# Optimization experiments

Measured on AMD Instinct MI355X. Metric: run time of the kernel, lower is better.

## Reference

```python
import jax, jax.numpy as jnp
import numpy as np

N = 50000      # nodes
E = 800000     # edges (before self-loops)
FIN = 512      # in_channels
HID = 64       # hid_units[i]
HEADS = 8      # n_heads[i]
OUT = 40       # out_channels
NEG_SLOPE = 0.2


def setup_inputs() -> dict:
    key = jax.random.key(0)
    ks = jax.random.split(key, 16)
    d = {
        "x": jax.random.normal(ks[0], (N, FIN), dtype=jnp.float32),
        "edge_index": jax.random.randint(ks[1], (2, E), 0, N, dtype=jnp.int64),
        # layer 1: FIN -> HEADS*HID
        "W1": jax.random.normal(ks[2], (FIN, HEADS * HID), dtype=jnp.float32) * 0.05,
        "att_src1": jax.random.normal(ks[3], (HEADS, HID), dtype=jnp.float32) * 0.1,
        "att_dst1": jax.random.normal(ks[4], (HEADS, HID), dtype=jnp.float32) * 0.1,
        "b1": jnp.zeros((HEADS * HID,), dtype=jnp.float32),
        # layer 2: HEADS*HID -> HEADS*HID
        "W2": jax.random.normal(ks[5], (HEADS * HID, HEADS * HID), dtype=jnp.float32) * 0.05,
        "att_src2": jax.random.normal(ks[6], (HEADS, HID), dtype=jnp.float32) * 0.1,
        "att_dst2": jax.random.normal(ks[7], (HEADS, HID), dtype=jnp.float32) * 0.1,
        "b2": jnp.zeros((HEADS * HID,), dtype=jnp.float32),
        # output layer: HEADS*HID -> OUT, 1 head, concat=False
        "W3": jax.random.normal(ks[8], (HEADS * HID, OUT), dtype=jnp.float32) * 0.05,
        "att_src3": jax.random.normal(ks[9], (1, OUT), dtype=jnp.float32) * 0.1,
        "att_dst3": jax.random.normal(ks[10], (1, OUT), dtype=jnp.float32) * 0.1,
        "b3": jnp.zeros((OUT,), dtype=jnp.float32),
    }
    return d


def gat_conv(x, src, dst, W, a_src, a_dst, b, heads, out_ch, concat):
    # x: [N, Fin]; src/dst: [E'] (self-loops included)
    h = (x @ W).reshape(N, heads, out_ch)              # [N, H, C]
    alpha_src = jnp.sum(h * a_src[None], axis=-1)      # [N, H]
    alpha_dst = jnp.sum(h * a_dst[None], axis=-1)      # [N, H]
    e = jax.nn.leaky_relu(alpha_src[src] + alpha_dst[dst], NEG_SLOPE)  # [E', H]
    # segment softmax over edges grouped by target node
    m = jax.ops.segment_max(e, dst, num_segments=N)    # [N, H]
    ex = jnp.exp(e - m[dst])
    denom = jax.ops.segment_sum(ex, dst, num_segments=N)
    alpha = ex / denom[dst]                            # [E', H]
    out = jax.ops.segment_sum(h[src] * alpha[:, :, None], dst, num_segments=N)  # [N, H, C]
    out = out.reshape(N, heads * out_ch) if concat else out.mean(axis=1)
    return out + b


def reference(x, edge_index, W1, att_src1, att_dst1, b1,
              W2, att_src2, att_dst2, b2,
              W3, att_src3, att_dst3, b3):
    loop = jnp.arange(N, dtype=edge_index.dtype)
    src = jnp.concatenate([edge_index[0], loop])  # add_self_loops=True (PyG default)
    dst = jnp.concatenate([edge_index[1], loop])
    h = gat_conv(x, src, dst, W1, att_src1, att_dst1, b1, HEADS, HID, True)
    h = jax.nn.elu(h)  # dropout p=0.0 / eval -> identity
    h = gat_conv(h, src, dst, W2, att_src2, att_dst2, b2, HEADS, HID, True)
    h = jax.nn.elu(h)
    h = gat_conv(h, src, dst, W3, att_src3, att_dst3, b3, 1, OUT, False)
    return jax.nn.log_softmax(h, axis=1)
```

## Files before the change

### kernel.cpp

```cpp
#include <hip/hip_runtime.h>
#include <math.h>

#define NNODES 50000
#define NEDGES 800000
#define FINCH 512
#define HIDC 64
#define NHEADS 8
#define OUTC 40
#define NSLOPE 0.2f
#define NSB ((NNODES + 255) / 256)

typedef unsigned short ushort;
typedef unsigned int uint;
typedef __attribute__((ext_vector_type(8))) short bf16x8;
typedef __attribute__((ext_vector_type(4))) float f32x4;

static __device__ __forceinline__ float leaky(float e) { return e > 0.f ? e : NSLOPE * e; }

static __device__ __forceinline__ float bf2f(ushort u) {
    union { unsigned int i; float f; } c; c.i = ((unsigned int)u) << 16; return c.f;
}
static __device__ __forceinline__ ushort f2bf(float f) {
    union { float f; unsigned int i; } c; c.f = f;
    unsigned int r = c.i + 0x7FFF + ((c.i >> 16) & 1);
    return (ushort)(r >> 16);
}
static __device__ __forceinline__ uint fkey(float f) {
    uint u = __float_as_uint(f);
    return (u & 0x80000000u) ? ~u : (u | 0x80000000u);
}
static __device__ __forceinline__ float fdec(uint k) {
    return __uint_as_float((k & 0x80000000u) ? (k & 0x7fffffffu) : ~k);
}

static __device__ __forceinline__ void gload16(const ushort* g, ushort* l) {
    __builtin_amdgcn_global_load_lds((const __attribute__((address_space(1))) void*)g,
                                     (__attribute__((address_space(3))) void*)l, 16, 0, 0);
}

__global__ __launch_bounds__(64) void k_detect(const int* __restrict__ ei, int* __restrict__ flag,
                                               uint* __restrict__ keys) {
    int lane = threadIdx.x;
    if (lane < 17) keys[lane] = fkey(-3.0e38f);
    int v = ei[2 * lane + 1];
    unsigned long long b = __ballot(v != 0);
    if (lane == 0) *flag = (b == 0ULL) ? 1 : 0;
}

static __device__ __forceinline__ int load_idx(const int* ei, int wide, int pos) {
    int v = wide ? ei[2 * (long long)pos] : ei[pos];
    v = v < 0 ? 0 : (v >= NNODES ? NNODES - 1 : v);
    return v;
}

__global__ void k_init_deg(int* __restrict__ deg) {
    int i = blockIdx.x * blockDim.x + threadIdx.x;
    if (i < NNODES) deg[i] = 1;
}

__global__ void k_count(const int* __restrict__ ei, const int* __restrict__ flag, int* __restrict__ deg) {
    int e = blockIdx.x * blockDim.x + threadIdx.x;
    if (e < NEDGES) {
        int d = load_idx(ei, *flag, NEDGES + e);
        atomicAdd(&deg[d], 1);
    }
}

__global__ __launch_bounds__(256) void k_bsum(const int* __restrict__ deg, int* __restrict__ bsum) {
    int i = blockIdx.x * 256 + threadIdx.x;
    int v = (i < NNODES) ? deg[i] : 0;
#pragma unroll
    for (int m = 32; m > 0; m >>= 1) v += __shfl_xor(v, m);
    __shared__ int ws[4];
    int wid = threadIdx.x >> 6, lane = threadIdx.x & 63;
    if (lane == 0) ws[wid] = v;
    __syncthreads();
    if (threadIdx.x == 0) bsum[blockIdx.x] = ws[0] + ws[1] + ws[2] + ws[3];
}

__global__ __launch_bounds__(64) void k_bscan(const int* __restrict__ bsum, int* __restrict__ bofs,
                                              int* __restrict__ offs) {
    const int lane = threadIdx.x;
    const int CH = (NSB + 63) / 64;
    int lo = lane * CH, hi = min(lo + CH, NSB);
    int s = 0;
    for (int i = lo; i < hi; i++) s += bsum[i];
    int x = s;
#pragma unroll
    for (int st = 1; st < 64; st <<= 1) { int v = __shfl_up(x, st); if (lane >= st) x += v; }
    int run = x - s;
    for (int i = lo; i < hi; i++) { bofs[i] = run; run += bsum[i]; }
    if (lane == 63) offs[NNODES] = run;
}

__global__ __launch_bounds__(256) void k_scan_final(const int* __restrict__ deg, const int* __restrict__ bofs,
                                                    int* __restrict__ offs, int* __restrict__ cur) {
    int b = blockIdx.x;
    int i = b * 256 + threadIdx.x;
    int v = (i < NNODES) ? deg[i] : 0;
    int lane = threadIdx.x & 63, wid = threadIdx.x >> 6;
    int x = v;
#pragma unroll
    for (int st = 1; st < 64; st <<= 1) { int t = __shfl_up(x, st); if (lane >= st) x += t; }
    __shared__ int ws[4];
    if (lane == 63) ws[wid] = x;
    __syncthreads();
    int wofs = 0;
#pragma unroll
    for (int w = 0; w < 4; w++) if (w < wid) wofs += ws[w];
    int excl = bofs[b] + wofs + x - v;
    if (i < NNODES) { offs[i] = excl; cur[i] = excl; }
}

__global__ void k_fill(const int* __restrict__ ei, const int* __restrict__ flag,
                       int* __restrict__ cur, int* __restrict__ csr) {
    int e = blockIdx.x * blockDim.x + threadIdx.x;
    if (e < NEDGES + NNODES) {
        int s, d;
        if (e < NEDGES) {
            int w = *flag;
            s = load_idx(ei, w, e);
            d = load_idx(ei, w, NEDGES + e);
        } else {
            s = e - NEDGES; d = s;
        }
        int pos = atomicAdd(&cur[d], 1);
        csr[pos] = s;
    }
}

template <int NH>
__global__ __launch_bounds__(256) void k_msrc(const float* __restrict__ src, uint* __restrict__ keys, int n) {
    float m = -3.0e38f;
    for (int i = blockIdx.x * 256 + threadIdx.x; i < n; i += gridDim.x * 256)
        m = fmaxf(m, src[i]);
    __shared__ float red[256];
    red[threadIdx.x] = m;
    __syncthreads();
    for (int st = 128; st >= NH; st >>= 1) {
        if (threadIdx.x < st) red[threadIdx.x] = fmaxf(red[threadIdx.x], red[threadIdx.x + st]);
        __syncthreads();
    }
    if (threadIdx.x < NH) atomicMax(&keys[threadIdx.x], fkey(red[threadIdx.x]));
}

__global__ void k_f2bf(const float* __restrict__ in, ushort* __restrict__ out, int n4) {
    int i = blockIdx.x * blockDim.x + threadIdx.x;
    if (i < n4) {
        float4 v = ((const float4*)in)[i];
        ushort4 o = make_ushort4(f2bf(v.x), f2bf(v.y), f2bf(v.z), f2bf(v.w));
        ((ushort4*)out)[i] = o;
    }
}

__global__ __launch_bounds__(256) void k_transpose(const float* __restrict__ W, ushort* __restrict__ Wt) {
    __shared__ float tile[32][33];
    int bx = blockIdx.x, by = blockIdx.y;
    int tx = threadIdx.x & 31, ty = threadIdx.x >> 5;
#pragma unroll
    for (int i = 0; i < 4; i++)
        tile[ty + i * 8][tx] = W[(size_t)(by * 32 + ty + i * 8) * 512 + bx * 32 + tx];
    __syncthreads();
#pragma unroll
    for (int i = 0; i < 4; i++)
        Wt[(size_t)(bx * 32 + ty + i * 8) * 512 + by * 32 + tx] = f2bf(tile[tx][ty + i * 8]);
}

__global__ __launch_bounds__(256) void k_transpose3(const float* __restrict__ W3, ushort* __restrict__ Wt3) {
    int idx = blockIdx.x * 256 + threadIdx.x;
    int c = idx >> 9, k = idx & 511;
    Wt3[idx] = (c < OUTC) ? f2bf(W3[(size_t)k * OUTC + c]) : 0;
}

__global__ __launch_bounds__(512) void mfma_gemm2(const ushort* __restrict__ A, const ushort* __restrict__ Bt,
                                                  ushort* __restrict__ C, int M) {
    __shared__ ushort Abuf[2][128 * 32];
    __shared__ ushort Bbuf[2][128 * 32];
    const int nwg = gridDim.x;
    const int q = nwg >> 3, r = nwg & 7;
    const int orig = blockIdx.x;
    const int xcd = orig & 7, ii = orig >> 3;
    const int wgid = (xcd < r ? xcd * (q + 1) : r * (q + 1) + (xcd - r) * q) + ii;
    const int row0 = (wgid >> 2) * 128, col0 = (wgid & 3) * 128;

    const int t = threadIdx.x;
    const int wid = t >> 6, lane = t & 63;
    const int wr = wid >> 1, wc = wid & 1;
    const int l15 = lane & 15, l4 = lane >> 4;
    const int arow = t >> 2, kb = t & 3;
    const int swz = (arow >> 1) & 3;
    const int ra = min(row0 + arow, M - 1);
    const ushort* gA = A + (size_t)ra * 512 + ((kb ^ swz) << 3);
    const ushort* gB = Bt + (size_t)(col0 + arow) * 512 + ((kb ^ swz) << 3);
    f32x4 acc[2][4] = {};

    gload16(gA, &Abuf[0][wid * 512]);
    gload16(gB, &Bbuf[0][wid * 512]);
    __syncthreads();
    int cur = 0;
    for (int k0 = 0; k0 < 512; k0 += 32) {
        if (k0 + 32 < 512) {
            gload16(gA + k0 + 32, &Abuf[cur ^ 1][wid * 512]);
            gload16(gB + k0 + 32, &Bbuf[cur ^ 1][wid * 512]);
        }
        bf16x8 af[2], bfr[4];
#pragma unroll
        for (int mr = 0; mr < 2; mr++) {
            int rr = wr * 32 + mr * 16 + l15;
            af[mr] = *(const bf16x8*)&Abuf[cur][rr * 32 + ((l4 ^ ((rr >> 1) & 3)) << 3)];
        }
#pragma unroll
        for (int nr = 0; nr < 4; nr++) {
            int cc = wc * 64 + nr * 16 + l15;
            bfr[nr] = *(const bf16x8*)&Bbuf[cur][cc * 32 + ((l4 ^ ((cc >> 1) & 3)) << 3)];
        }
#pragma unroll
        for (int mr = 0; mr < 2; mr++)
#pragma unroll
            for (int nr = 0; nr < 4; nr++)
                acc[mr][nr] = __builtin_amdgcn_mfma_f32_16x16x32_bf16(af[mr], bfr[nr], acc[mr][nr], 0, 0, 0);
        __syncthreads();
        cur ^= 1;
    }
#pragma unroll
    for (int mr = 0; mr < 2; mr++) {
#pragma unroll
        for (int qq = 0; qq < 4; qq++) {
            int gr = row0 + wr * 32 + mr * 16 + l4 * 4 + qq;
            if (gr >= M) continue;
#pragma unroll
            for (int nr = 0; nr < 4; nr++) {
                int gc = col0 + wc * 64 + nr * 16 + l15;
                C[(size_t)gr * 512 + gc] = f2bf(acc[mr][nr][qq]);
            }
        }
    }
}

__global__ __launch_bounds__(256) void mfma_gemm3(const ushort* __restrict__ A, const ushort* __restrict__ Wt3,
                                                  float* __restrict__ h3, int M) {
    __shared__ ushort Abuf[2][64 * 32];
    __shared__ ushort Bbuf[2][64 * 32];
    const int t = threadIdx.x;
    const int wid = t >> 6, lane = t & 63;
    const int row0 = blockIdx.x * 64;
    const int l15 = lane & 15, l4 = lane >> 4;
    const int arow = t >> 2, kb = t & 3;
    const int swz = (arow >> 1) & 3;
    const int ra = min(row0 + arow, M - 1);
    const ushort* gA = A + (size_t)ra * 512 + ((kb ^ swz) << 3);
    const ushort* gB = Wt3 + (size_t)arow * 512 + ((kb ^ swz) << 3);
    f32x4 acc[4] = {};
    gload16(gA, &Abuf[0][wid * 512]);
    gload16(gB, &Bbuf[0][wid * 512]);
    __syncthreads();
    int cur = 0;
    for (int k0 = 0; k0 < 512; k0 += 32) {
        if (k0 + 32 < 512) {
            gload16(gA + k0 + 32, &Abuf[cur ^ 1][wid * 512]);
            gload16(gB + k0 + 32, &Bbuf[cur ^ 1][wid * 512]);
        }
        int rr = wid * 16 + l15;
        bf16x8 af = *(const bf16x8*)&Abuf[cur][rr * 32 + ((l4 ^ ((rr >> 1) & 3)) << 3)];
        bf16x8 bfr[4];
#pragma unroll
        for (int nr = 0; nr < 4; nr++) {
            int cc = nr * 16 + l15;
            bfr[nr] = *(const bf16x8*)&Bbuf[cur][cc * 32 + ((l4 ^ ((cc >> 1) & 3)) << 3)];
        }
#pragma unroll
        for (int nr = 0; nr < 4; nr++)
            acc[nr] = __builtin_amdgcn_mfma_f32_16x16x32_bf16(af, bfr[nr], acc[nr], 0, 0, 0);
        __syncthreads();
        cur ^= 1;
    }
#pragma unroll
    for (int qq = 0; qq < 4; qq++) {
        int gr = row0 + wid * 16 + l4 * 4 + qq;
        if (gr >= M) continue;
#pragma unroll
        for (int nr = 0; nr < 4; nr++) {
            int c = nr * 16 + l15;
            if (c < OUTC) h3[(size_t)gr * OUTC + c] = acc[nr][qq];
        }
    }
}

__global__ __launch_bounds__(256) void k_alpha8(const ushort* __restrict__ h, const float* __restrict__ att_s,
                                                const float* __restrict__ att_d, float* __restrict__ asrc,
                                                float* __restrict__ adst) {
    int gw = (blockIdx.x * 256 + threadIdx.x) >> 6;
    int lane = threadIdx.x & 63;
    if (gw >= NNODES * NHEADS) return;
    int n = gw >> 3, hh = gw & 7;
    float v = bf2f(h[(size_t)n * FINCH + hh * HIDC + lane]);
    float s1 = v * att_s[hh * HIDC + lane];
    float s2 = v * att_d[hh * HIDC + lane];
#pragma unroll
    for (int m = 32; m > 0; m >>= 1) { s1 += __shfl_xor(s1, m); s2 += __shfl_xor(s2, m); }
    if (lane == 0) { asrc[n * 8 + hh] = s1; adst[n * 8 + hh] = s2; }
}

__global__ __launch_bounds__(256) void k_alpha1(const float* __restrict__ h, const float* __restrict__ att_s,
                                                const float* __restrict__ att_d, float* __restrict__ asrc,
                                                float* __restrict__ adst) {
    int gw = (blockIdx.x * 256 + threadIdx.x) >> 6;
    int lane = threadIdx.x & 63;
    if (gw >= NNODES) return;
    float s1 = 0.f, s2 = 0.f;
    if (lane < OUTC) {
        float v = h[(size_t)gw * OUTC + lane];
        s1 = v * att_s[lane];
        s2 = v * att_d[lane];
    }
#pragma unroll
    for (int m = 32; m > 0; m >>= 1) { s1 += __shfl_xor(s1, m); s2 += __shfl_xor(s2, m); }
    if (lane == 0) { asrc[gw] = s1; adst[gw] = s2; }
}

template <bool DO_ELU>
__global__ __launch_bounds__(256) void agg_v4(const ushort* __restrict__ h, const float* __restrict__ asrc,
                                              const float* __restrict__ adst, const int* __restrict__ offs,
                                              const int* __restrict__ csr, const float* __restrict__ bias,
                                              const uint* __restrict__ mkeys, ushort* __restrict__ out) {
    const int wid = threadIdx.x >> 6, lane = threadIdx.x & 63;
    const int n = blockIdx.x * 4 + wid;
    if (n >= NNODES) return;
    const int beg = offs[n], deg = offs[n + 1] - beg;
    const int h8 = lane & 7;
    const int es = lane >> 3;
    const float ad_s = adst[n * 8 + h8];
    const float m8 = leaky(fdec(mkeys[h8]) + ad_s);

    float ss = 0.f;
    for (int i = es; i < deg; i += 8) {
        int s = csr[beg + i];
        ss += expf(leaky(asrc[s * 8 + h8] + ad_s) - m8);
    }
    ss += __shfl_xor(ss, 8);
    ss += __shfl_xor(ss, 16);
    ss += __shfl_xor(ss, 32);
    const float rs8 = 1.f / ss;

    const int hc = lane >> 3;
    float acc[8] = {0.f, 0.f, 0.f, 0.f, 0.f, 0.f, 0.f, 0.f};
    int base = 0;
    for (; base + 8 <= deg; base += 8) {
        int sv = csr[beg + base + es];
        float wv = expf(leaky(asrc[sv * 8 + h8] + ad_s) - m8) * rs8;
#pragma unroll
        for (int j = 0; j < 8; j++) {
            int src = (j << 3) | hc;
            float w = __shfl(wv, src);
            int s = __shfl(sv, src);
            bf16x8 hv = *(const bf16x8*)(h + (size_t)s * FINCH + lane * 8);
#pragma unroll
            for (int c = 0; c < 8; c++) acc[c] = fmaf(bf2f((ushort)hv[c]), w, acc[c]);
        }
    }
    if (base < deg) {
        int e = base + es;
        int sv = csr[beg + min(e, deg - 1)];
        float wv = (e < deg) ? expf(leaky(asrc[sv * 8 + h8] + ad_s) - m8) * rs8 : 0.f;
        int cnt = deg - base;
        for (int j = 0; j < cnt; j++) {
            int src = (j << 3) | hc;
            float w = __shfl(wv, src);
            int s = __shfl(sv, src);
            bf16x8 hv = *(const bf16x8*)(h + (size_t)s * FINCH + lane * 8);
#pragma unroll
            for (int c = 0; c < 8; c++) acc[c] = fmaf(bf2f((ushort)hv[c]), w, acc[c]);
        }
    }
    ushort o[8];
#pragma unroll
    for (int c = 0; c < 8; c++) {
        float v = acc[c] + bias[lane * 8 + c];
        if (DO_ELU) v = v > 0.f ? v : expf(v) - 1.f;
        o[c] = f2bf(v);
    }
    *(bf16x8*)(out + (size_t)n * FINCH + lane * 8) = *(bf16x8*)o;
}

__global__ __launch_bounds__(64) void agg_out(const float* __restrict__ h3, const float* __restrict__ asrc,
                                              const float* __restrict__ adst, const int* __restrict__ offs,
                                              const int* __restrict__ csr, const float* __restrict__ bias,
                                              const uint* __restrict__ mkeys, float* __restrict__ out) {
    const int n = blockIdx.x, lane = threadIdx.x;
    const int beg = offs[n], deg = offs[n + 1] - beg;
    const float ad = adst[n];
    const float m = leaky(fdec(mkeys[0]) + ad);

    float ss = 0.f;
    for (int i = lane; i < deg; i += 64) ss += expf(leaky(asrc[csr[beg + i]] + ad) - m);
#pragma unroll
    for (int w = 32; w > 0; w >>= 1) ss += __shfl_xor(ss, w);
    float rs = 1.f / ss;

    float acc = 0.f;
    for (int base = 0; base < deg; base += 64) {
        int sv = (base + lane < deg) ? csr[beg + base + lane] : 0;
        int cnt = min(64, deg - base);
        int j = 0;
        for (; j + 2 <= cnt; j += 2) {
            int s0 = __shfl(sv, j), s1 = __shfl(sv, j + 1);
            float a0 = asrc[s0], a1 = asrc[s1];
            float v0 = (lane < OUTC) ? h3[(size_t)s0 * OUTC + lane] : 0.f;
            float v1 = (lane < OUTC) ? h3[(size_t)s1 * OUTC + lane] : 0.f;
            float w0 = expf(leaky(a0 + ad) - m) * rs;
            float w1 = expf(leaky(a1 + ad) - m) * rs;
            acc = fmaf(v0, w0, acc);
            acc = fmaf(v1, w1, acc);
        }
        if (j < cnt) {
            int s0 = __shfl(sv, j);
            float w0 = expf(leaky(asrc[s0] + ad) - m) * rs;
            float v0 = (lane < OUTC) ? h3[(size_t)s0 * OUTC + lane] : 0.f;
            acc = fmaf(v0, w0, acc);
        }
    }
    float v = (lane < OUTC) ? acc + bias[lane] : -1e30f;
    float mx = v;
#pragma unroll
    for (int w = 32; w > 0; w >>= 1) mx = fmaxf(mx, __shfl_xor(mx, w));
    float ex = (lane < OUTC) ? expf(v - mx) : 0.f;
    float se = ex;
#pragma unroll
    for (int w = 32; w > 0; w >>= 1) se += __shfl_xor(se, w);
    if (lane < OUTC) out[(size_t)n * OUTC + lane] = v - mx - logf(se);
}

extern "C" void kernel_launch(void* const* d_in, const int* in_sizes, int n_in,
                              void* d_out, int out_size, void* d_ws, size_t ws_size,
                              hipStream_t stream) {
    const float* x   = (const float*)d_in[0];
    const int*   ei  = (const int*)d_in[1];
    const float* W1  = (const float*)d_in[2];
    const float* as1 = (const float*)d_in[3];
    const float* ad1 = (const float*)d_in[4];
    const float* b1  = (const float*)d_in[5];
    const float* W2  = (const float*)d_in[6];
    const float* as2 = (const float*)d_in[7];
    const float* ad2 = (const float*)d_in[8];
    const float* b2  = (const float*)d_in[9];
    const float* W3  = (const float*)d_in[10];
    const float* as3 = (const float*)d_in[11];
    const float* ad3 = (const float*)d_in[12];
    const float* b3  = (const float*)d_in[13];
    float* out = (float*)d_out;

    char* p = (char*)d_ws;
    ushort* bufA = (ushort*)p; p += (size_t)NNODES * FINCH * 2;
    ushort* bufB = (ushort*)p; p += (size_t)NNODES * FINCH * 2;
    float* asrc = (float*)p; p += (size_t)NNODES * 8 * 4;
    float* adst = (float*)p; p += (size_t)NNODES * 8 * 4;
    int* flag = (int*)p; p += 16;
    uint* mkeys = (uint*)p; p += 128;
    int* deg  = (int*)p; p += (size_t)NNODES * 4;
    int* offs = (int*)p; p += (size_t)(NNODES + 1) * 4;
    int* cur  = (int*)p; p += (size_t)NNODES * 4;
    int* csr  = (int*)p; p += (size_t)(NEDGES + NNODES) * 4;
    ushort* Wt1 = (ushort*)p; p += (size_t)512 * 512 * 2;
    ushort* Wt2 = (ushort*)p; p += (size_t)512 * 512 * 2;
    ushort* Wt3 = (ushort*)p; p += (size_t)64 * 512 * 2;
    int* bsum = (int*)p; p += (size_t)NSB * 4;
    int* bofs = (int*)p; p += (size_t)NSB * 4;
    float* h3 = (float*)bufA;
    float* asc3 = asrc;
    float* adc3 = adst;

    k_detect<<<1, 64, 0, stream>>>(ei, flag, mkeys);
    k_init_deg<<<(NNODES + 255) / 256, 256, 0, stream>>>(deg);
    k_count<<<(NEDGES + 255) / 256, 256, 0, stream>>>(ei, flag, deg);
    k_bsum<<<NSB, 256, 0, stream>>>(deg, bsum);
    k_bscan<<<1, 64, 0, stream>>>(bsum, bofs, offs);
    k_scan_final<<<NSB, 256, 0, stream>>>(deg, bofs, offs, cur);
    k_fill<<<(NEDGES + NNODES + 255) / 256, 256, 0, stream>>>(ei, flag, cur, csr);

    {
        int n4 = NNODES * FINCH / 4;
        k_f2bf<<<(n4 + 255) / 256, 256, 0, stream>>>(x, bufB, n4);
        dim3 gt(16, 16);
        k_transpose<<<gt, 256, 0, stream>>>(W1, Wt1);
        k_transpose<<<gt, 256, 0, stream>>>(W2, Wt2);
        k_transpose3<<<128, 256, 0, stream>>>(W3, Wt3);
    }

    int nwg = 4 * ((NNODES + 127) / 128);
    int gagg = (NNODES + 3) / 4;
    mfma_gemm2<<<nwg, 512, 0, stream>>>(bufB, Wt1, bufA, NNODES);
    k_alpha8<<<(NNODES * 8 * 64) / 256, 256, 0, stream>>>(bufA, as1, ad1, asrc, adst);
    k_msrc<8><<<128, 256, 0, stream>>>(asrc, mkeys, NNODES * 8);
    agg_v4<true><<<gagg, 256, 0, stream>>>(bufA, asrc, adst, offs, csr, b1, mkeys, bufB);
    mfma_gemm2<<<nwg, 512, 0, stream>>>(bufB, Wt2, bufA, NNODES);
    k_alpha8<<<(NNODES * 8 * 64) / 256, 256, 0, stream>>>(bufA, as2, ad2, asrc, adst);
    k_msrc<8><<<128, 256, 0, stream>>>(asrc, mkeys + 8, NNODES * 8);
    agg_v4<true><<<gagg, 256, 0, stream>>>(bufA, asrc, adst, offs, csr, b2, mkeys + 8, bufB);
    mfma_gemm3<<<(NNODES + 63) / 64, 256, 0, stream>>>(bufB, Wt3, h3, NNODES);
    k_alpha1<<<(NNODES * 64 + 255) / 256, 256, 0, stream>>>(h3, as3, ad3, asc3, adc3);
    k_msrc<1><<<128, 256, 0, stream>>>(asc3, mkeys + 16, NNODES);
    agg_out<<<NNODES, 64, 0, stream>>>(h3, asc3, adc3, offs, csr, b3, mkeys + 16, out);
}
```

Measured before the change: 685.4 us.

## Fuse attention logits into GEMM epilogue and store layer-1 features as FP8

Computes the per-head source/destination attention logits inside the MFMA GEMM epilogue from the fp32 accumulators, which removes the separate k_alpha8 kernels and their re-read of the feature matrix. For layer 1, it also stores the transformed features as FP8 (when the compiler exposes the conversion builtins) and adds an FP8 aggregation kernel, halving gather bytes in the bandwidth-bound edge aggregation. The FP8 store writes single bytes per lane, which may give less efficient store coalescing, and FP8 storage reduces numerical precision of layer-1 features, risking tolerance failures.

```diff
diff --git a/kernel.cpp b/kernel.cpp
--- a/kernel.cpp
+++ b/kernel.cpp
@@ -12,8 +12,16 @@
 
 typedef unsigned short ushort;
 typedef unsigned int uint;
+typedef unsigned char uchar;
 typedef __attribute__((ext_vector_type(8))) short bf16x8;
 typedef __attribute__((ext_vector_type(4))) float f32x4;
+typedef __attribute__((ext_vector_type(2))) float f32x2;
+
+#if __has_builtin(__builtin_amdgcn_cvt_pk_f32_fp8) && __has_builtin(__builtin_amdgcn_cvt_pk_fp8_f32)
+#define HAS_FP8 1
+#else
+#define HAS_FP8 0
+#endif
 
 static __device__ __forceinline__ float leaky(float e) { return e > 0.f ? e : NSLOPE * e; }
 
@@ -172,8 +180,11 @@
     Wt3[idx] = (c < OUTC) ? f2bf(W3[(size_t)k * OUTC + c]) : 0;
 }
 
+template <int CMODE>
 __global__ __launch_bounds__(512) void mfma_gemm2(const ushort* __restrict__ A, const ushort* __restrict__ Bt,
-                                                  ushort* __restrict__ C, int M) {
+                                                  void* __restrict__ Cv,
+                                                  const float* __restrict__ att_s, const float* __restrict__ att_d,
+                                                  float* __restrict__ asrc, float* __restrict__ adst, int M) {
     __shared__ ushort Abuf[2][128 * 32];
     __shared__ ushort Bbuf[2][128 * 32];
     const int nwg = gridDim.x;
@@ -231,8 +242,41 @@
 #pragma unroll
             for (int nr = 0; nr < 4; nr++) {
                 int gc = col0 + wc * 64 + nr * 16 + l15;
-                C[(size_t)gr * 512 + gc] = f2bf(acc[mr][nr][qq]);
+                if (CMODE == 0) {
+                    ((ushort*)Cv)[(size_t)gr * 512 + gc] = f2bf(acc[mr][nr][qq]);
+                } else {
+#if HAS_FP8
+                    uint pk = __builtin_amdgcn_cvt_pk_fp8_f32(acc[mr][nr][qq], acc[mr][nr][qq], 0, false);
+                    ((uchar*)Cv)[(size_t)gr * 512 + gc] = (uchar)(pk & 0xff);
+#endif
+                }
             }
+        }
+    }
+    const int hd = ((wgid & 3) << 1) | wc;
+    float asf[4], adf[4];
+#pragma unroll
+    for (int nr = 0; nr < 4; nr++) {
+        asf[nr] = att_s[hd * 64 + nr * 16 + l15];
+        adf[nr] = att_d[hd * 64 + nr * 16 + l15];
+    }
+#pragma unroll
+    for (int mr = 0; mr < 2; mr++) {
+#pragma unroll
+        for (int qq = 0; qq < 4; qq++) {
+            float s1 = 0.f, s2 = 0.f;
+#pragma unroll
+            for (int nr = 0; nr < 4; nr++) {
+                s1 = fmaf(acc[mr][nr][qq], asf[nr], s1);
+                s2 = fmaf(acc[mr][nr][qq], adf[nr], s2);
+            }
+#pragma unroll
+            for (int st = 1; st < 16; st <<= 1) {
+                s1 += __shfl_xor(s1, st);
+                s2 += __shfl_xor(s2, st);
+            }
+            int gr = row0 + wr * 32 + mr * 16 + l4 * 4 + qq;
+            if (gr < M && l15 == 0) { asrc[gr * 8 + hd] = s1; adst[gr * 8 + hd] = s2; }
         }
     }
 }
@@ -286,21 +330,6 @@
     }
 }
 
-__global__ __launch_bounds__(256) void k_alpha8(const ushort* __restrict__ h, const float* __restrict__ att_s,
-                                                const float* __restrict__ att_d, float* __restrict__ asrc,
-                                                float* __restrict__ adst) {
-    int gw = (blockIdx.x * 256 + threadIdx.x) >> 6;
-    int lane = threadIdx.x & 63;
-    if (gw >= NNODES * NHEADS) return;
-    int n = gw >> 3, hh = gw & 7;
-    float v = bf2f(h[(size_t)n * FINCH + hh * HIDC + lane]);
-    float s1 = v * att_s[hh * HIDC + lane];
-    float s2 = v * att_d[hh * HIDC + lane];
-#pragma unroll
-    for (int m = 32; m > 0; m >>= 1) { s1 += __shfl_xor(s1, m); s2 += __shfl_xor(s2, m); }
-    if (lane == 0) { asrc[n * 8 + hh] = s1; adst[n * 8 + hh] = s2; }
-}
-
 __global__ __launch_bounds__(256) void k_alpha1(const float* __restrict__ h, const float* __restrict__ att_s,
                                                 const float* __restrict__ att_d, float* __restrict__ asrc,
                                                 float* __restrict__ adst) {
@@ -381,6 +410,84 @@
     }
     *(bf16x8*)(out + (size_t)n * FINCH + lane * 8) = *(bf16x8*)o;
 }
+
+#if HAS_FP8
+template <bool DO_ELU>
+__global__ __launch_bounds__(256) void agg_v5(const uchar* __restrict__ h, const float* __restrict__ asrc,
+                                              const float* __restrict__ adst, const int* __restrict__ offs,
+                                              const int* __restrict__ csr, const float* __restrict__ bias,
+                                              const uint* __restrict__ mkeys, ushort* __restrict__ out) {
+    const int wid = threadIdx.x >> 6, lane = threadIdx.x & 63;
+    const int n = blockIdx.x * 4 + wid;
+    if (n >= NNODES) return;
+    const int beg = offs[n], deg = offs[n + 1] - beg;
+    const int h8 = lane & 7;
+    const int es = lane >> 3;
+    const float ad_s = adst[n * 8 + h8];
+    const float m8 = leaky(fdec(mkeys[h8]) + ad_s);
+
+    float ss = 0.f;
+    for (int i = es; i < deg; i += 8) {
+        int s = csr[beg + i];
+        ss += expf(leaky(asrc[s * 8 + h8] + ad_s) - m8);
+    }
+    ss += __shfl_xor(ss, 8);
+    ss += __shfl_xor(ss, 16);
+    ss += __shfl_xor(ss, 32);
+    const float rs8 = 1.f / ss;
+
+    const int hc = lane >> 3;
+    float acc[8] = {0.f, 0.f, 0.f, 0.f, 0.f, 0.f, 0.f, 0.f};
+    int base = 0;
+    for (; base + 8 <= deg; base += 8) {
+        int sv = csr[beg + base + es];
+        float wv = expf(leaky(asrc[sv * 8 + h8] + ad_s) - m8) * rs8;
+#pragma unroll
+        for (int j = 0; j < 8; j++) {
+            int src = (j << 3) | hc;
+            float w = __shfl(wv, src);
+            int s = __shfl(sv, src);
+            uint2 u = *(const uint2*)(h + (size_t)s * 512 + lane * 8);
+            f32x2 p0 = __builtin_amdgcn_cvt_pk_f32_fp8(u.x, false);
+            f32x2 p1 = __builtin_amdgcn_cvt_pk_f32_fp8(u.x, true);
+            f32x2 p2 = __builtin_amdgcn_cvt_pk_f32_fp8(u.y, false);
+            f32x2 p3 = __builtin_amdgcn_cvt_pk_f32_fp8(u.y, true);
+            acc[0] = fmaf(p0[0], w, acc[0]); acc[1] = fmaf(p0[1], w, acc[1]);
+            acc[2] = fmaf(p1[0], w, acc[2]); acc[3] = fmaf(p1[1], w, acc[3]);
+            acc[4] = fmaf(p2[0], w, acc[4]); acc[5] = fmaf(p2[1], w, acc[5]);
+            acc[6] = fmaf(p3[0], w, acc[6]); acc[7] = fmaf(p3[1], w, acc[7]);
+        }
+    }
+    if (base < deg) {
+        int e = base + es;
+        int sv = csr[beg + min(e, deg - 1)];
+        float wv = (e < deg) ? expf(leaky(asrc[sv * 8 + h8] + ad_s) - m8) * rs8 : 0.f;
+        int cnt = deg - base;
+        for (int j = 0; j < cnt; j++) {
+            int src = (j << 3) | hc;
+            float w = __shfl(wv, src);
+            int s = __shfl(sv, src);
+            uint2 u = *(const uint2*)(h + (size_t)s * 512 + lane * 8);
+            f32x2 p0 = __builtin_amdgcn_cvt_pk_f32_fp8(u.x, false);
+            f32x2 p1 = __builtin_amdgcn_cvt_pk_f32_fp8(u.x, true);
+            f32x2 p2 = __builtin_amdgcn_cvt_pk_f32_fp8(u.y, false);
+            f32x2 p3 = __builtin_amdgcn_cvt_pk_f32_fp8(u.y, true);
+            acc[0] = fmaf(p0[0], w, acc[0]); acc[1] = fmaf(p0[1], w, acc[1]);
+            acc[2] = fmaf(p1[0], w, acc[2]); acc[3] = fmaf(p1[1], w, acc[3]);
+            acc[4] = fmaf(p2[0], w, acc[4]); acc[5] = fmaf(p2[1], w, acc[5]);
+            acc[6] = fmaf(p3[0], w, acc[6]); acc[7] = fmaf(p3[1], w, acc[7]);
+        }
+    }
+    ushort o[8];
+#pragma unroll
+    for (int c = 0; c < 8; c++) {
+        float v = acc[c] + bias[lane * 8 + c];
+        if (DO_ELU) v = v > 0.f ? v : expf(v) - 1.f;
+        o[c] = f2bf(v);
+    }
+    *(bf16x8*)(out + (size_t)n * FINCH + lane * 8) = *(bf16x8*)o;
+}
+#endif
 
 __global__ __launch_bounds__(64) void agg_out(const float* __restrict__ h3, const float* __restrict__ asrc,
                                               const float* __restrict__ adst, const int* __restrict__ offs,
@@ -488,12 +595,16 @@
 
     int nwg = 4 * ((NNODES + 127) / 128);
     int gagg = (NNODES + 3) / 4;
-    mfma_gemm2<<<nwg, 512, 0, stream>>>(bufB, Wt1, bufA, NNODES);
-    k_alpha8<<<(NNODES * 8 * 64) / 256, 256, 0, stream>>>(bufA, as1, ad1, asrc, adst);
+#if HAS_FP8
+    mfma_gemm2<1><<<nwg, 512, 0, stream>>>(bufB, Wt1, bufA, as1, ad1, asrc, adst, NNODES);
+    k_msrc<8><<<128, 256, 0, stream>>>(asrc, mkeys, NNODES * 8);
+    agg_v5<true><<<gagg, 256, 0, stream>>>((const uchar*)bufA, asrc, adst, offs, csr, b1, mkeys, bufB);
+#else
+    mfma_gemm2<0><<<nwg, 512, 0, stream>>>(bufB, Wt1, bufA, as1, ad1, asrc, adst, NNODES);
     k_msrc<8><<<128, 256, 0, stream>>>(asrc, mkeys, NNODES * 8);
     agg_v4<true><<<gagg, 256, 0, stream>>>(bufA, asrc, adst, offs, csr, b1, mkeys, bufB);
-    mfma_gemm2<<<nwg, 512, 0, stream>>>(bufB, Wt2, bufA, NNODES);
-    k_alpha8<<<(NNODES * 8 * 64) / 256, 256, 0, stream>>>(bufA, as2, ad2, asrc, adst);
+#endif
+    mfma_gemm2<0><<<nwg, 512, 0, stream>>>(bufB, Wt2, bufA, as2, ad2, asrc, adst, NNODES);
     k_msrc<8><<<128, 256, 0, stream>>>(asrc, mkeys + 8, NNODES * 8);
     agg_v4<true><<<gagg, 256, 0, stream>>>(bufA, asrc, adst, offs, csr, b2, mkeys + 8, bufB);
     mfma_gemm3<<<(NNODES + 63) / 64, 256, 0, stream>>>(bufB, Wt3, h3, NNODES);
```

Measured after the change: 597.2 us, median of 3. 12.9% less time.
